# Performance work log

Hardware: AMD Instinct MI355X
Metric: run time of the kernel (lower is better)

## Reference

```python
import jax, jax.numpy as jnp
import numpy as np

D = 256
NUM_STAB = 1024
NUM_CYCLES = 128
B, S = 64, 4096
EPS = 1e-5


def setup_inputs() -> dict:
    key = jax.random.key(0)
    ks = jax.random.split(key, 32)
    inp = {
        'meas': jax.random.normal(ks[0], (B, S), jnp.float32),
        'event': jax.random.normal(ks[1], (B, S), jnp.float32),
        'leak': jax.random.uniform(ks[2], (B, S), jnp.float32),
        'event_leak': jax.random.uniform(ks[3], (B, S), jnp.float32),
        'stab_ids': jax.random.randint(ks[4], (B, S), 0, NUM_STAB),
        'cycle_ids': jax.random.randint(ks[5], (B, S), 0, NUM_CYCLES),
        # Linear(1, d): weight is a length-d vector, plus bias
        'w_meas': jax.random.normal(ks[6], (D,), jnp.float32) * 0.02,
        'b_meas': jnp.zeros((D,), jnp.float32),
        'w_event': jax.random.normal(ks[7], (D,), jnp.float32) * 0.02,
        'b_event': jnp.zeros((D,), jnp.float32),
        'w_leak': jax.random.normal(ks[8], (D,), jnp.float32) * 0.02,
        'b_leak': jnp.zeros((D,), jnp.float32),
        'w_el': jax.random.normal(ks[9], (D,), jnp.float32) * 0.02,
        'b_el': jnp.zeros((D,), jnp.float32),
        'stab_table': jax.random.normal(ks[10], (NUM_STAB, D), jnp.float32) * 0.02,
        'cycle_table': jax.random.normal(ks[11], (NUM_CYCLES, D), jnp.float32) * 0.02,
        # res block 1
        'g1': jnp.ones((D,), jnp.float32),
        'be1': jnp.zeros((D,), jnp.float32),
        'W11': jax.random.normal(ks[12], (D, D), jnp.float32) * (1.0 / np.sqrt(D)),
        'b11': jnp.zeros((D,), jnp.float32),
        'W12': jax.random.normal(ks[13], (D, D), jnp.float32) * (1.0 / np.sqrt(D)),
        'b12': jnp.zeros((D,), jnp.float32),
        # res block 2
        'g2': jnp.ones((D,), jnp.float32),
        'be2': jnp.zeros((D,), jnp.float32),
        'W21': jax.random.normal(ks[14], (D, D), jnp.float32) * (1.0 / np.sqrt(D)),
        'b21': jnp.zeros((D,), jnp.float32),
        'W22': jax.random.normal(ks[15], (D, D), jnp.float32) * (1.0 / np.sqrt(D)),
        'b22': jnp.zeros((D,), jnp.float32),
    }
    return inp


def _layernorm(x, g, b):
    mu = jnp.mean(x, axis=-1, keepdims=True)
    var = jnp.mean(jnp.square(x - mu), axis=-1, keepdims=True)
    return (x - mu) * jax.lax.rsqrt(var + EPS) * g + b


def _res_block(x, g, be, W1, b1, W2, b2):
    h = _layernorm(x, g, be)
    h = jax.nn.gelu(h @ W1 + b1, approximate=False)  # torch F.gelu default = exact erf
    return x + h @ W2 + b2


def reference(meas, event, leak, event_leak, stab_ids, cycle_ids,
              w_meas, b_meas, w_event, b_event, w_leak, b_leak, w_el, b_el,
              stab_table, cycle_table,
              g1, be1, W11, b11, W12, b12,
              g2, be2, W21, b21, W22, b22):
    # Linear(1,d)(x.unsqueeze(-1)) == x[...,None]*w + b; fuse the four projections.
    h = (meas[..., None] * w_meas + b_meas
         + event[..., None] * w_event + b_event
         + leak[..., None] * w_leak + b_leak
         + event_leak[..., None] * w_el + b_el
         + stab_table[stab_ids]
         + cycle_table[cycle_ids])  # (B, S, D)
    h = _res_block(h, g1, be1, W11, b11, W12, b12)
    h = _res_block(h, g2, be2, W21, b21, W22, b22)
    return h
```

## Files before the change

kernel.cpp:

```cpp
#include <hip/hip_runtime.h>

#define NTOK 262144
#define TT 64
#define EPS 1e-5f

typedef short short8 __attribute__((ext_vector_type(8)));
typedef float float4v __attribute__((ext_vector_type(4)));

__device__ __align__(16) short g_Wp[4 * 65536];

__device__ __forceinline__ short f2bf(float f) {
    uint32_t u = __builtin_bit_cast(uint32_t, f);
    u += 0x7FFFu + ((u >> 16) & 1u);
    return (short)(u >> 16);
}

__global__ void pack_w(const float* __restrict__ W11, const float* __restrict__ W12,
                       const float* __restrict__ W21, const float* __restrict__ W22) {
    int t = blockIdx.x * 256 + threadIdx.x;
    int g = t >> 16;
    int r = t & 65535;
    int j = r & 7, l = (r >> 3) & 63, kb = (r >> 9) & 7, nt = (r >> 12) & 15;
    int n = nt * 16 + (l & 15);
    int k = kb * 32 + (l >> 4) * 8 + j;
    const float* W = (g == 0) ? W11 : (g == 1) ? W12 : (g == 2) ? W21 : W22;
    g_Wp[t] = f2bf(W[k * 256 + n]);
}

__device__ __forceinline__ float gelu_erf(float v) {
    float z = fabsf(v) * 0.70710678118654752f;
    float d = __builtin_fmaf(0.3275911f, z, 1.0f);
    float t;
    asm("v_rcp_f32 %0, %1" : "=v"(t) : "v"(d));
    float poly = t * (0.254829592f + t * (-0.284496736f + t * (1.421413741f
               + t * (-1.453152027f + t * 1.061405429f))));
    float er = 1.0f - poly * __expf(-z * z);
    er = copysignf(er, v);
    return 0.5f * v * (1.0f + er);
}

__device__ __forceinline__ int aidx(int m, int k) {
    int lp = (m & 15) | (((k >> 3) & 3) << 4);
    int gs = (lp >> 2) | ((lp & 3) << 4);
    return ((((m >> 4) * 8 + (k >> 5)) * 64) + gs) * 8 + (k & 7);
}

__global__ __launch_bounds__(256, 1) void fused_kernel(
    const float* __restrict__ meas, const float* __restrict__ event,
    const float* __restrict__ leak, const float* __restrict__ elk,
    const int* __restrict__ sids, const int* __restrict__ cids,
    const float* __restrict__ w_meas, const float* __restrict__ w_event,
    const float* __restrict__ w_leak, const float* __restrict__ w_el,
    const float* __restrict__ b_meas, const float* __restrict__ b_event,
    const float* __restrict__ b_leak, const float* __restrict__ b_el,
    const float* __restrict__ stab_table, const float* __restrict__ cycle_table,
    const float* __restrict__ g1, const float* __restrict__ be1,
    const float* __restrict__ b11, const float* __restrict__ b12,
    const float* __restrict__ g2, const float* __restrict__ be2,
    const float* __restrict__ b21, const float* __restrict__ b22,
    float* __restrict__ out)
{
    __shared__ __align__(16) short Abuf[4 * 8 * 64 * 8];
    __shared__ float par[13 * 256];
    __shared__ __align__(16) float ubuf[768];

    float (*rowf)[TT] = (float (*)[TT])ubuf;
    int   (*rowi)[TT] = (int (*)[TT])(ubuf + 256);
    float *redp = ubuf;

    const int tid = threadIdx.x;
    const int w = tid >> 6, lane = tid & 63;
    const int q = lane >> 4, c = lane & 15;
    const int gl = (lane >> 2) | ((lane & 3) << 4);
    const int R0 = blockIdx.x * TT;

    {
        int n = tid;
        par[0 * 256 + n] = w_meas[n];
        par[1 * 256 + n] = w_event[n];
        par[2 * 256 + n] = w_leak[n];
        par[3 * 256 + n] = w_el[n];
        par[4 * 256 + n] = b_meas[n] + b_event[n] + b_leak[n] + b_el[n];
        par[5 * 256 + n] = g1[n];
        par[6 * 256 + n] = be1[n];
        par[7 * 256 + n] = b11[n];
        par[8 * 256 + n] = b12[n];
        par[9 * 256 + n] = g2[n];
        par[10 * 256 + n] = be2[n];
        par[11 * 256 + n] = b21[n];
        par[12 * 256 + n] = b22[n];
    }
    if (tid < TT) {
        rowf[0][tid] = meas[R0 + tid];
        rowf[1][tid] = event[R0 + tid];
        rowf[2][tid] = leak[R0 + tid];
        rowf[3][tid] = elk[R0 + tid];
        rowi[0][tid] = sids[R0 + tid];
        rowi[1][tid] = cids[R0 + tid];
    }
    __syncthreads();

    float xr[4][4][4];
    #pragma unroll
    for (int rg = 0; rg < 4; ++rg)
        #pragma unroll
        for (int reg = 0; reg < 4; ++reg) {
            int m = rg * 16 + 4 * q + reg;
            float mv = rowf[0][m], ev = rowf[1][m], lv = rowf[2][m], e2 = rowf[3][m];
            const float* srow = stab_table + rowi[0][m] * 256;
            const float* crow = cycle_table + rowi[1][m] * 256;
            #pragma unroll
            for (int ntl = 0; ntl < 4; ++ntl) {
                int n = w * 64 + ntl * 16 + c;
                xr[rg][ntl][reg] = mv * par[n] + ev * par[256 + n] + lv * par[512 + n]
                                 + e2 * par[768 + n] + par[1024 + n] + srow[n] + crow[n];
            }
        }
    __syncthreads();

    float4v acc[4][4];

    auto ln_reduce = [&]() {
        float s[4][4], s2[4][4];
        #pragma unroll
        for (int rg = 0; rg < 4; ++rg)
            #pragma unroll
            for (int reg = 0; reg < 4; ++reg) {
                float a = 0.f, b = 0.f;
                #pragma unroll
                for (int ntl = 0; ntl < 4; ++ntl) {
                    float v = xr[rg][ntl][reg];
                    a += v; b += v * v;
                }
                #pragma unroll
                for (int d = 1; d < 16; d <<= 1) {
                    a += __shfl_xor(a, d, 64);
                    b += __shfl_xor(b, d, 64);
                }
                s[rg][reg] = a; s2[rg][reg] = b;
            }
        if (c == 0) {
            #pragma unroll
            for (int rg = 0; rg < 4; ++rg)
                #pragma unroll
                for (int reg = 0; reg < 4; ++reg) {
                    int m = rg * 16 + 4 * q + reg;
                    redp[m * 12 + w] = s[rg][reg];
                    redp[m * 12 + 4 + w] = s2[rg][reg];
                }
        }
    };

    auto ln_write = [&](const float* g, const float* be, short* A) {
        float gv[4], bv[4];
        #pragma unroll
        for (int ntl = 0; ntl < 4; ++ntl) {
            int n = w * 64 + ntl * 16 + c;
            gv[ntl] = g[n]; bv[ntl] = be[n];
        }
        #pragma unroll
        for (int rg = 0; rg < 4; ++rg)
            #pragma unroll
            for (int reg = 0; reg < 4; ++reg) {
                int m = rg * 16 + 4 * q + reg;
                float4v a4 = *(const float4v*)&redp[m * 12];
                float4v b4 = *(const float4v*)&redp[m * 12 + 4];
                float a = a4[0] + a4[1] + a4[2] + a4[3];
                float b = b4[0] + b4[1] + b4[2] + b4[3];
                float mu = a * (1.0f / 256.0f);
                float ve = b * (1.0f / 256.0f) - mu * mu + EPS;
                float rs;
                asm("v_rsq_f32 %0, %1" : "=v"(rs) : "v"(ve));
                #pragma unroll
                for (int ntl = 0; ntl < 4; ++ntl) {
                    int n = w * 64 + ntl * 16 + c;
                    A[aidx(m, n)] = f2bf((xr[rg][ntl][reg] - mu) * rs * gv[ntl] + bv[ntl]);
                }
            }
    };

    auto preB = [&](int g4, short8 bh0[4]) {
        const short* W = g_Wp + g4 * 65536;
        #pragma unroll
        for (int ntl = 0; ntl < 4; ++ntl) {
            int nt = w * 4 + ntl;
            bh0[ntl] = *(const short8*)&W[((nt * 8 + 0) * 64 + lane) * 8];
        }
    };

    auto do_gemm = [&](int g4, const short* A, const short8 bh0[4]) {
        const short* W = g_Wp + g4 * 65536;
        #pragma unroll
        for (int rg = 0; rg < 4; ++rg)
            #pragma unroll
            for (int ntl = 0; ntl < 4; ++ntl)
                acc[rg][ntl] = (float4v){0.f, 0.f, 0.f, 0.f};
        short8 ah[2][4], bh[2][4];
        #pragma unroll
        for (int rg = 0; rg < 4; ++rg)
            ah[0][rg] = *(const short8*)&A[((rg * 8 + 0) * 64 + gl) * 8];
        #pragma unroll
        for (int ntl = 0; ntl < 4; ++ntl)
            bh[0][ntl] = bh0[ntl];
        #pragma unroll
        for (int kb = 0; kb < 8; ++kb) {
            const int cur = kb & 1, nxt = cur ^ 1;
            if (kb < 7) {
                #pragma unroll
                for (int rg = 0; rg < 4; ++rg)
                    ah[nxt][rg] = *(const short8*)&A[((rg * 8 + kb + 1) * 64 + gl) * 8];
                #pragma unroll
                for (int ntl = 0; ntl < 4; ++ntl) {
                    int nt = w * 4 + ntl;
                    bh[nxt][ntl] = *(const short8*)&W[((nt * 8 + kb + 1) * 64 + lane) * 8];
                }
            }
            __builtin_amdgcn_s_setprio(1);
            #pragma unroll
            for (int rg = 0; rg < 4; ++rg)
                #pragma unroll
                for (int ntl = 0; ntl < 4; ++ntl)
                    acc[rg][ntl] = __builtin_amdgcn_mfma_f32_16x16x32_bf16(
                        ah[cur][rg], bh[cur][ntl], acc[rg][ntl], 0, 0, 0);
            __builtin_amdgcn_s_setprio(0);
        }
    };

    auto gelu_write = [&](const float* bias, short* A) {
        float bv[4];
        #pragma unroll
        for (int ntl = 0; ntl < 4; ++ntl)
            bv[ntl] = bias[w * 64 + ntl * 16 + c];
        #pragma unroll
        for (int rg = 0; rg < 4; ++rg)
            #pragma unroll
            for (int ntl = 0; ntl < 4; ++ntl)
                #pragma unroll
                for (int reg = 0; reg < 4; ++reg) {
                    int m = rg * 16 + 4 * q + reg;
                    int n = w * 64 + ntl * 16 + c;
                    A[aidx(m, n)] = f2bf(gelu_erf(acc[rg][ntl][reg] + bv[ntl]));
                }
    };

    short* A = Abuf;
    short8 bh0[4];

    ln_reduce();
    __syncthreads();
    preB(0, bh0);
    ln_write(par + 5 * 256, par + 6 * 256, A);
    __syncthreads();
    do_gemm(0, A, bh0);
    preB(1, bh0);
    __syncthreads();
    gelu_write(par + 7 * 256, A);
    __syncthreads();
    do_gemm(1, A, bh0);
    {
        float bv[4];
        #pragma unroll
        for (int ntl = 0; ntl < 4; ++ntl)
            bv[ntl] = par[8 * 256 + w * 64 + ntl * 16 + c];
        #pragma unroll
        for (int rg = 0; rg < 4; ++rg)
            #pragma unroll
            for (int ntl = 0; ntl < 4; ++ntl)
                #pragma unroll
                for (int reg = 0; reg < 4; ++reg)
                    xr[rg][ntl][reg] += acc[rg][ntl][reg] + bv[ntl];
    }

    ln_reduce();
    __syncthreads();
    preB(2, bh0);
    ln_write(par + 9 * 256, par + 10 * 256, A);
    __syncthreads();
    do_gemm(2, A, bh0);
    preB(3, bh0);
    __syncthreads();
    gelu_write(par + 11 * 256, A);
    __syncthreads();
    do_gemm(3, A, bh0);

    {
        float bv[4];
        #pragma unroll
        for (int ntl = 0; ntl < 4; ++ntl)
            bv[ntl] = par[12 * 256 + w * 64 + ntl * 16 + c];
        #pragma unroll
        for (int rg = 0; rg < 4; ++rg)
            #pragma unroll
            for (int ntl = 0; ntl < 4; ++ntl)
                #pragma unroll
                for (int reg = 0; reg < 4; ++reg) {
                    int m = rg * 16 + 4 * q + reg;
                    int n = w * 64 + ntl * 16 + c;
                    out[(size_t)(R0 + m) * 256 + n] =
                        xr[rg][ntl][reg] + acc[rg][ntl][reg] + bv[ntl];
                }
    }
}

extern "C" void kernel_launch(void* const* d_in, const int* in_sizes, int n_in,
                              void* d_out, int out_size, void* d_ws, size_t ws_size,
                              hipStream_t stream) {
    pack_w<<<1024, 256, 0, stream>>>(
        (const float*)d_in[18], (const float*)d_in[20],
        (const float*)d_in[24], (const float*)d_in[26]);
    fused_kernel<<<NTOK / TT, 256, 0, stream>>>(
        (const float*)d_in[0], (const float*)d_in[1],
        (const float*)d_in[2], (const float*)d_in[3],
        (const int*)d_in[4], (const int*)d_in[5],
        (const float*)d_in[6], (const float*)d_in[8],
        (const float*)d_in[10], (const float*)d_in[12],
        (const float*)d_in[7], (const float*)d_in[9],
        (const float*)d_in[11], (const float*)d_in[13],
        (const float*)d_in[14], (const float*)d_in[15],
        (const float*)d_in[16], (const float*)d_in[17],
        (const float*)d_in[19], (const float*)d_in[21],
        (const float*)d_in[22], (const float*)d_in[23],
        (const float*)d_in[25], (const float*)d_in[27],
        (float*)d_out);
}
```

Baseline: 671.1 us.

## Run two token tiles per block in staggered phases to overlap GEMM with elementwise

Each block now holds 512 threads in two 4-wave halves, each with its own 64-token tile and its own A and reduction buffers in shared memory. The halves run the same stage sequence offset by one phase, separated by block-wide barriers, so one half's MFMA GEMM runs alongside the other half's layernorm or GELU work. The aim is to fill the matrix units while the vector/transcendental stages run, instead of serializing them inside a single 256-thread block. The cost is more barriers per tile, twice the shared memory per block, and register pressure from the 512-thread launch bound.

```diff
diff --git a/kernel.cpp b/kernel.cpp
--- a/kernel.cpp
+++ b/kernel.cpp
@@ -45,7 +45,7 @@
     return ((((m >> 4) * 8 + (k >> 5)) * 64) + gs) * 8 + (k & 7);
 }
 
-__global__ __launch_bounds__(256, 1) void fused_kernel(
+__global__ __launch_bounds__(512, 1) void fused_kernel(
     const float* __restrict__ meas, const float* __restrict__ event,
     const float* __restrict__ leak, const float* __restrict__ elk,
     const int* __restrict__ sids, const int* __restrict__ cids,
@@ -60,21 +60,25 @@
     const float* __restrict__ b21, const float* __restrict__ b22,
     float* __restrict__ out)
 {
-    __shared__ __align__(16) short Abuf[4 * 8 * 64 * 8];
+    __shared__ __align__(16) short Abuf[2][4 * 8 * 64 * 8];
     __shared__ float par[13 * 256];
-    __shared__ __align__(16) float ubuf[768];
-
-    float (*rowf)[TT] = (float (*)[TT])ubuf;
-    int   (*rowi)[TT] = (int (*)[TT])(ubuf + 256);
-    float *redp = ubuf;
+    __shared__ __align__(16) float ubuf[2][768];
 
     const int tid = threadIdx.x;
-    const int w = tid >> 6, lane = tid & 63;
+    const int w = tid >> 6;
+    const int half = w >> 2;
+    const int wh = w & 3;
+    const int lane = tid & 63;
     const int q = lane >> 4, c = lane & 15;
     const int gl = (lane >> 2) | ((lane & 3) << 4);
-    const int R0 = blockIdx.x * TT;
-
-    {
+    const int R0h = blockIdx.x * 2 * TT + half * TT;
+
+    float (*rowf)[TT] = (float (*)[TT])ubuf[half];
+    int   (*rowi)[TT] = (int (*)[TT])(ubuf[half] + 256);
+    float *redp = ubuf[half];
+    short *Ah = Abuf[half];
+
+    if (tid < 256) {
         int n = tid;
         par[0 * 256 + n] = w_meas[n];
         par[1 * 256 + n] = w_event[n];
@@ -90,13 +94,16 @@
         par[11 * 256 + n] = b21[n];
         par[12 * 256 + n] = b22[n];
     }
-    if (tid < TT) {
-        rowf[0][tid] = meas[R0 + tid];
-        rowf[1][tid] = event[R0 + tid];
-        rowf[2][tid] = leak[R0 + tid];
-        rowf[3][tid] = elk[R0 + tid];
-        rowi[0][tid] = sids[R0 + tid];
-        rowi[1][tid] = cids[R0 + tid];
+    {
+        int th = tid & 255;
+        if (th < TT) {
+            rowf[0][th] = meas[R0h + th];
+            rowf[1][th] = event[R0h + th];
+            rowf[2][th] = leak[R0h + th];
+            rowf[3][th] = elk[R0h + th];
+            rowi[0][th] = sids[R0h + th];
+            rowi[1][th] = cids[R0h + th];
+        }
     }
     __syncthreads();
 
@@ -111,7 +118,7 @@
             const float* crow = cycle_table + rowi[1][m] * 256;
             #pragma unroll
             for (int ntl = 0; ntl < 4; ++ntl) {
-                int n = w * 64 + ntl * 16 + c;
+                int n = wh * 64 + ntl * 16 + c;
                 xr[rg][ntl][reg] = mv * par[n] + ev * par[256 + n] + lv * par[512 + n]
                                  + e2 * par[768 + n] + par[1024 + n] + srow[n] + crow[n];
             }
@@ -145,17 +152,17 @@
                 #pragma unroll
                 for (int reg = 0; reg < 4; ++reg) {
                     int m = rg * 16 + 4 * q + reg;
-                    redp[m * 12 + w] = s[rg][reg];
-                    redp[m * 12 + 4 + w] = s2[rg][reg];
-                }
-        }
-    };
-
-    auto ln_write = [&](const float* g, const float* be, short* A) {
+                    redp[m * 12 + wh] = s[rg][reg];
+                    redp[m * 12 + 4 + wh] = s2[rg][reg];
+                }
+        }
+    };
+
+    auto ln_write = [&](const float* g, const float* be) {
         float gv[4], bv[4];
         #pragma unroll
         for (int ntl = 0; ntl < 4; ++ntl) {
-            int n = w * 64 + ntl * 16 + c;
+            int n = wh * 64 + ntl * 16 + c;
             gv[ntl] = g[n]; bv[ntl] = be[n];
         }
         #pragma unroll
@@ -173,22 +180,23 @@
                 asm("v_rsq_f32 %0, %1" : "=v"(rs) : "v"(ve));
                 #pragma unroll
                 for (int ntl = 0; ntl < 4; ++ntl) {
-                    int n = w * 64 + ntl * 16 + c;
-                    A[aidx(m, n)] = f2bf((xr[rg][ntl][reg] - mu) * rs * gv[ntl] + bv[ntl]);
+                    int n = wh * 64 + ntl * 16 + c;
+                    Ah[aidx(m, n)] = f2bf((xr[rg][ntl][reg] - mu) * rs * gv[ntl] + bv[ntl]);
                 }
             }
     };
 
-    auto preB = [&](int g4, short8 bh0[4]) {
+    short8 bh0[4];
+    auto preB = [&](int g4) {
         const short* W = g_Wp + g4 * 65536;
         #pragma unroll
         for (int ntl = 0; ntl < 4; ++ntl) {
-            int nt = w * 4 + ntl;
+            int nt = wh * 4 + ntl;
             bh0[ntl] = *(const short8*)&W[((nt * 8 + 0) * 64 + lane) * 8];
         }
     };
 
-    auto do_gemm = [&](int g4, const short* A, const short8 bh0[4]) {
+    auto do_gemm = [&](int g4) {
         const short* W = g_Wp + g4 * 65536;
         #pragma unroll
         for (int rg = 0; rg < 4; ++rg)
@@ -198,7 +206,7 @@
         short8 ah[2][4], bh[2][4];
         #pragma unroll
         for (int rg = 0; rg < 4; ++rg)
-            ah[0][rg] = *(const short8*)&A[((rg * 8 + 0) * 64 + gl) * 8];
+            ah[0][rg] = *(const short8*)&Ah[((rg * 8 + 0) * 64 + gl) * 8];
         #pragma unroll
         for (int ntl = 0; ntl < 4; ++ntl)
             bh[0][ntl] = bh0[ntl];
@@ -208,10 +216,10 @@
             if (kb < 7) {
                 #pragma unroll
                 for (int rg = 0; rg < 4; ++rg)
-                    ah[nxt][rg] = *(const short8*)&A[((rg * 8 + kb + 1) * 64 + gl) * 8];
+                    ah[nxt][rg] = *(const short8*)&Ah[((rg * 8 + kb + 1) * 64 + gl) * 8];
                 #pragma unroll
                 for (int ntl = 0; ntl < 4; ++ntl) {
-                    int nt = w * 4 + ntl;
+                    int nt = wh * 4 + ntl;
                     bh[nxt][ntl] = *(const short8*)&W[((nt * 8 + kb + 1) * 64 + lane) * 8];
                 }
             }
@@ -226,11 +234,11 @@
         }
     };
 
-    auto gelu_write = [&](const float* bias, short* A) {
+    auto gelu_write = [&](const float* bias) {
         float bv[4];
         #pragma unroll
         for (int ntl = 0; ntl < 4; ++ntl)
-            bv[ntl] = bias[w * 64 + ntl * 16 + c];
+            bv[ntl] = bias[wh * 64 + ntl * 16 + c];
         #pragma unroll
         for (int rg = 0; rg < 4; ++rg)
             #pragma unroll
@@ -238,30 +246,16 @@
                 #pragma unroll
                 for (int reg = 0; reg < 4; ++reg) {
                     int m = rg * 16 + 4 * q + reg;
-                    int n = w * 64 + ntl * 16 + c;
-                    A[aidx(m, n)] = f2bf(gelu_erf(acc[rg][ntl][reg] + bv[ntl]));
-                }
-    };
-
-    short* A = Abuf;
-    short8 bh0[4];
-
-    ln_reduce();
-    __syncthreads();
-    preB(0, bh0);
-    ln_write(par + 5 * 256, par + 6 * 256, A);
-    __syncthreads();
-    do_gemm(0, A, bh0);
-    preB(1, bh0);
-    __syncthreads();
-    gelu_write(par + 7 * 256, A);
-    __syncthreads();
-    do_gemm(1, A, bh0);
-    {
+                    int n = wh * 64 + ntl * 16 + c;
+                    Ah[aidx(m, n)] = f2bf(gelu_erf(acc[rg][ntl][reg] + bv[ntl]));
+                }
+    };
+
+    auto resadd = [&]() {
         float bv[4];
         #pragma unroll
         for (int ntl = 0; ntl < 4; ++ntl)
-            bv[ntl] = par[8 * 256 + w * 64 + ntl * 16 + c];
+            bv[ntl] = par[8 * 256 + wh * 64 + ntl * 16 + c];
         #pragma unroll
         for (int rg = 0; rg < 4; ++rg)
             #pragma unroll
@@ -269,25 +263,13 @@
                 #pragma unroll
                 for (int reg = 0; reg < 4; ++reg)
                     xr[rg][ntl][reg] += acc[rg][ntl][reg] + bv[ntl];
-    }
-
-    ln_reduce();
-    __syncthreads();
-    preB(2, bh0);
-    ln_write(par + 9 * 256, par + 10 * 256, A);
-    __syncthreads();
-    do_gemm(2, A, bh0);
-    preB(3, bh0);
-    __syncthreads();
-    gelu_write(par + 11 * 256, A);
-    __syncthreads();
-    do_gemm(3, A, bh0);
-
-    {
+    };
+
+    auto store_out = [&]() {
         float bv[4];
         #pragma unroll
         for (int ntl = 0; ntl < 4; ++ntl)
-            bv[ntl] = par[12 * 256 + w * 64 + ntl * 16 + c];
+            bv[ntl] = par[12 * 256 + wh * 64 + ntl * 16 + c];
         #pragma unroll
         for (int rg = 0; rg < 4; ++rg)
             #pragma unroll
@@ -295,11 +277,36 @@
                 #pragma unroll
                 for (int reg = 0; reg < 4; ++reg) {
                     int m = rg * 16 + 4 * q + reg;
-                    int n = w * 64 + ntl * 16 + c;
-                    out[(size_t)(R0 + m) * 256 + n] =
+                    int n = wh * 64 + ntl * 16 + c;
+                    out[(size_t)(R0h + m) * 256 + n] =
                         xr[rg][ntl][reg] + acc[rg][ntl][reg] + bv[ntl];
                 }
-    }
+    };
+
+    if (!half) ln_reduce();
+    __syncthreads();
+    if (!half) { preB(0); ln_write(par + 5*256, par + 6*256); } else ln_reduce();
+    __syncthreads();
+    if (!half) do_gemm(0); else { preB(0); ln_write(par + 5*256, par + 6*256); }
+    __syncthreads();
+    if (!half) { preB(1); gelu_write(par + 7*256); } else do_gemm(0);
+    __syncthreads();
+    if (!half) do_gemm(1); else { preB(1); gelu_write(par + 7*256); }
+    __syncthreads();
+    if (!half) resadd(); else do_gemm(1);
+    __syncthreads();
+    if (!half) ln_reduce(); else resadd();
+    __syncthreads();
+    if (!half) { preB(2); ln_write(par + 9*256, par + 10*256); } else ln_reduce();
+    __syncthreads();
+    if (!half) do_gemm(2); else { preB(2); ln_write(par + 9*256, par + 10*256); }
+    __syncthreads();
+    if (!half) { preB(3); gelu_write(par + 11*256); } else do_gemm(2);
+    __syncthreads();
+    if (!half) do_gemm(3); else { preB(3); gelu_write(par + 11*256); }
+    __syncthreads();
+    if (!half) store_out(); else do_gemm(3);
+    if (half) store_out();
 }
 
 extern "C" void kernel_launch(void* const* d_in, const int* in_sizes, int n_in,
@@ -308,7 +315,7 @@
     pack_w<<<1024, 256, 0, stream>>>(
         (const float*)d_in[18], (const float*)d_in[20],
         (const float*)d_in[24], (const float*)d_in[26]);
-    fused_kernel<<<NTOK / TT, 256, 0, stream>>>(
+    fused_kernel<<<NTOK / (2 * TT), 512, 0, stream>>>(
         (const float*)d_in[0], (const float*)d_in[1],
         (const float*)d_in[2], (const float*)d_in[3],
         (const int*)d_in[4], (const int*)d_in[5],
```

Measured after the change: 608.5 us. 1.1x faster.
